# Performance work log

Hardware: AMD Instinct MI355X
Metric: run time of the kernel (lower is better)

## Reference

```python
import jax, jax.numpy as jnp
import numpy as np

EPS = 1e-8  # matches torch F.cosine_similarity eps


def setup_inputs() -> dict:
    key = jax.random.key(0)
    k1, k2 = jax.random.split(key)
    num_nodes, feat_dim, num_edges = 100000, 128, 1600000
    node_features = jax.random.normal(k1, (num_nodes, feat_dim), dtype=jnp.float32)
    edge_index = jax.random.randint(k2, (2, num_edges), 0, num_nodes, dtype=jnp.int64)
    return {"node_features": node_features, "edge_index": edge_index}


def reference(node_features, edge_index):
    # Edge-parallel equivalent of the per-node loop:
    # each edge (s, d) contributes cos(u_s, u_d) to BOTH s and d
    # (the original adj dict appends both directions, duplicates included).
    num_nodes = node_features.shape[0]
    src, dst = edge_index[0], edge_index[1]

    # clamped norms as in torch cosine_similarity
    norms = jnp.maximum(jnp.linalg.norm(node_features, axis=-1), EPS)  # [N]

    # per-edge cosine similarity  [E]
    sim = jnp.einsum("ed,ed->e", node_features[src], node_features[dst]) / (
        norms[src] * norms[dst]
    )

    idx = jnp.concatenate([src, dst])            # [2E] — both endpoints
    vals = jnp.concatenate([sim, sim])           # [2E]
    sums = jax.ops.segment_sum(vals, idx, num_segments=num_nodes)          # [N]
    deg = jax.ops.segment_sum(jnp.ones_like(vals), idx, num_segments=num_nodes)

    # isolated nodes get similarity 1.0
    return jnp.where(deg > 0, sums / jnp.maximum(deg, 1.0), 1.0)
```

## Files before the change

### kernel.cpp

```cpp
#include <hip/hip_runtime.h>

#define FEAT 128
#define NB 8
#define HB 256
#define CHN 25000
#define CNT_SHIFT 24
#define SIM_SCALE 16384.0f
#define INV_SIM (1.0f/16384.0f)

typedef unsigned uv4 __attribute__((ext_vector_type(4)));
typedef unsigned short us4 __attribute__((ext_vector_type(4)));
typedef unsigned long long ull;

__device__ __forceinline__ int dot4(unsigned a, unsigned b, int c) {
#if __has_builtin(__builtin_amdgcn_sdot4)
    return __builtin_amdgcn_sdot4(a, b, c, false);
#else
    c += (int)(signed char)(a)        * (int)(signed char)(b);
    c += (int)(signed char)(a >> 8)   * (int)(signed char)(b >> 8);
    c += (int)(signed char)(a >> 16)  * (int)(signed char)(b >> 16);
    c += (int)(signed char)(a >> 24)  * (int)(signed char)(b >> 24);
    return c;
#endif
}

__device__ __forceinline__ int dot16(uv4 a, uv4 b) {
    int c = dot4(a.x, b.x, 0);
    c = dot4(a.y, b.y, c);
    c = dot4(a.z, b.z, c);
    return dot4(a.w, b.w, c);
}

__global__ void quantize_kernel(const float* __restrict__ feat,
                                unsigned* __restrict__ tab32,
                                float* __restrict__ invq,
                                int num_nodes) {
    const int sub = threadIdx.x & 31;
    const int hpb = blockDim.x >> 5;
    int n = blockIdx.x * hpb + (threadIdx.x >> 5);
    const int stride = gridDim.x * hpb;
    for (; n < num_nodes; n += stride) {
        const float4 v = *reinterpret_cast<const float4*>(feat + (size_t)n * FEAT + sub * 4);
        float am = fmaxf(fmaxf(fabsf(v.x), fabsf(v.y)), fmaxf(fabsf(v.z), fabsf(v.w)));
        am = fmaxf(am, __shfl_xor(am, 16, 64));
        am = fmaxf(am, __shfl_xor(am, 8, 64));
        am = fmaxf(am, __shfl_xor(am, 4, 64));
        am = fmaxf(am, __shfl_xor(am, 2, 64));
        am = fmaxf(am, __shfl_xor(am, 1, 64));
        const float sc = (am > 0.0f) ? (127.0f / am) : 0.0f;
        const int q0 = (int)rintf(v.x * sc);
        const int q1 = (int)rintf(v.y * sc);
        const int q2 = (int)rintf(v.z * sc);
        const int q3 = (int)rintf(v.w * sc);
        int nq = q0 * q0 + q1 * q1 + q2 * q2 + q3 * q3;
        nq += __shfl_xor(nq, 16, 64);
        nq += __shfl_xor(nq, 8, 64);
        nq += __shfl_xor(nq, 4, 64);
        nq += __shfl_xor(nq, 2, 64);
        nq += __shfl_xor(nq, 1, 64);
        tab32[(size_t)n * (FEAT / 4) + sub] =
            (unsigned)(q0 & 0xFF) | ((unsigned)(q1 & 0xFF) << 8) |
            ((unsigned)(q2 & 0xFF) << 16) | ((unsigned)(q3 & 0xFF) << 24);
        if (sub == 0)
            invq[n] = (nq > 0) ? (1.0f / sqrtf((float)nq)) : 0.0f;
    }
}

__global__ void hist_kernel(const int* __restrict__ ei,
                            unsigned* __restrict__ hist,
                            int num_edges, int slice, int chunk) {
    __shared__ unsigned h[NB];
    if (threadIdx.x < NB) h[threadIdx.x] = 0;
    __syncthreads();
    const int lo = blockIdx.x * chunk;
    const int hi = min(lo + chunk, num_edges);
    for (int e = lo + threadIdx.x; e < hi; e += blockDim.x)
        atomicAdd(&h[(unsigned)ei[e] / (unsigned)slice], 1u);
    __syncthreads();
    if (threadIdx.x < NB) hist[threadIdx.x * HB + blockIdx.x] = h[threadIdx.x];
}

__global__ void scan_kernel(unsigned* __restrict__ hist,
                            unsigned* __restrict__ qs,
                            int num_edges) {
    __shared__ unsigned part[256];
    const int t = threadIdx.x;
    unsigned v[8], sum = 0;
#pragma unroll
    for (int i = 0; i < 8; ++i) { v[i] = hist[t * 8 + i]; sum += v[i]; }
    part[t] = sum;
    __syncthreads();
    for (int off = 1; off < 256; off <<= 1) {
        const unsigned x = (t >= off) ? part[t - off] : 0u;
        __syncthreads();
        part[t] += x;
        __syncthreads();
    }
    unsigned run = part[t] - sum;
    if ((t & 31) == 0) qs[t >> 5] = run;
    if (t == 255) qs[NB] = part[255];
#pragma unroll
    for (int i = 0; i < 8; ++i) { const unsigned tmp = v[i]; hist[t * 8 + i] = run; run += tmp; }
}

__global__ void scatter_kernel(const int* __restrict__ ei,
                               const unsigned* __restrict__ hist,
                               ull* __restrict__ sd,
                               int num_edges, int slice, int chunk) {
    __shared__ unsigned cnt[NB];
    if (threadIdx.x < NB) cnt[threadIdx.x] = hist[threadIdx.x * HB + blockIdx.x];
    __syncthreads();
    const int lo = blockIdx.x * chunk;
    const int hi = min(lo + chunk, num_edges);
    for (int e = lo + threadIdx.x; e < hi; e += blockDim.x) {
        const unsigned s = (unsigned)ei[e];
        const unsigned d = (unsigned)ei[(size_t)num_edges + e];
        const unsigned pos = atomicAdd(&cnt[s / (unsigned)slice], 1u);
        sd[pos] = (ull)s | ((ull)d << 32);
    }
}

__global__ void edge_i8_flat_sd(const unsigned char* __restrict__ tab,
                                const ull* __restrict__ sd,
                                const float* __restrict__ invq,
                                unsigned short* __restrict__ sim,
                                int num_edges) {
    const int sub = threadIdx.x & 7;
    const int gid = blockIdx.x * (blockDim.x >> 3) + (threadIdx.x >> 3);
    const int e0 = gid * 4;
    if (e0 >= num_edges) return;
    const bool full = (e0 + 4 <= num_edges);

    int s[4], d[4];
    if (full) {
        const ulonglong2 w0 = *(const ulonglong2*)(sd + e0);
        const ulonglong2 w1 = *(const ulonglong2*)(sd + e0 + 2);
        s[0] = (int)(unsigned)w0.x; d[0] = (int)(unsigned)(w0.x >> 32);
        s[1] = (int)(unsigned)w0.y; d[1] = (int)(unsigned)(w0.y >> 32);
        s[2] = (int)(unsigned)w1.x; d[2] = (int)(unsigned)(w1.x >> 32);
        s[3] = (int)(unsigned)w1.y; d[3] = (int)(unsigned)(w1.y >> 32);
    } else {
#pragma unroll
        for (int k = 0; k < 4; ++k) {
            const int e = min(e0 + k, num_edges - 1);
            const ull w = sd[e];
            s[k] = (int)(unsigned)w; d[k] = (int)(unsigned)(w >> 32);
        }
    }

    uv4 a[4], b[4];
#pragma unroll
    for (int k = 0; k < 4; ++k) {
        a[k] = *(const uv4*)(tab + (size_t)s[k] * FEAT + sub * 16);
        b[k] = *(const uv4*)(tab + (size_t)d[k] * FEAT + sub * 16);
    }
    int pd[4];
#pragma unroll
    for (int k = 0; k < 4; ++k) pd[k] = dot16(a[k], b[k]);
#pragma unroll
    for (int k = 0; k < 4; ++k) {
        pd[k] += __shfl_xor(pd[k], 1, 64);
        pd[k] += __shfl_xor(pd[k], 2, 64);
        pd[k] += __shfl_xor(pd[k], 4, 64);
    }

    int myidx = s[0];
    if (sub == 1) myidx = d[0];
    else if (sub == 2) myidx = s[1];
    else if (sub == 3) myidx = d[1];
    else if (sub == 4) myidx = s[2];
    else if (sub == 5) myidx = d[2];
    else if (sub == 6) myidx = s[3];
    else if (sub == 7) myidx = d[3];

    const float msc = invq[myidx];
    const float prod = msc * __shfl_xor(msc, 1, 64);

    const int gb = (threadIdx.x & 63) & ~7;
    const float pr0 = __shfl(prod, gb + 0, 64);
    const float pr1 = __shfl(prod, gb + 2, 64);
    const float pr2 = __shfl(prod, gb + 4, 64);
    const float pr3 = __shfl(prod, gb + 6, 64);

    if (sub == 0) {
        us4 o;
        o.x = (unsigned short)((float)pd[0] * pr0 * SIM_SCALE + 32768.5f);
        o.y = (unsigned short)((float)pd[1] * pr1 * SIM_SCALE + 32768.5f);
        o.z = (unsigned short)((float)pd[2] * pr2 * SIM_SCALE + 32768.5f);
        o.w = (unsigned short)((float)pd[3] * pr3 * SIM_SCALE + 32768.5f);
        if (full) {
            *(us4*)(sim + e0) = o;
        } else {
            if (e0 < num_edges) sim[e0] = o.x;
            if (e0 + 1 < num_edges) sim[e0 + 1] = o.y;
            if (e0 + 2 < num_edges) sim[e0 + 2] = o.z;
            if (e0 + 3 < num_edges) sim[e0 + 3] = o.w;
        }
    }
}

__global__ void edge_i8_sim(const unsigned char* __restrict__ tab,
                            const int* __restrict__ ei,
                            const float* __restrict__ invq,
                            unsigned short* __restrict__ sim,
                            int num_edges, int aligned4) {
    const int sub = threadIdx.x & 7;
    const int gid = blockIdx.x * (blockDim.x >> 3) + (threadIdx.x >> 3);
    const int e0 = gid * 4;
    if (e0 >= num_edges) return;
    int s[4], d[4];
    const bool fast = aligned4 && (e0 + 4 <= num_edges);
    if (fast) {
        const uv4 si = *(const uv4*)(ei + e0);
        const uv4 di = *(const uv4*)(ei + (size_t)num_edges + e0);
        s[0] = (int)si.x; s[1] = (int)si.y; s[2] = (int)si.z; s[3] = (int)si.w;
        d[0] = (int)di.x; d[1] = (int)di.y; d[2] = (int)di.z; d[3] = (int)di.w;
    } else {
#pragma unroll
        for (int k = 0; k < 4; ++k) {
            const int e = min(e0 + k, num_edges - 1);
            s[k] = ei[e];
            d[k] = ei[(size_t)num_edges + e];
        }
    }
    uv4 a[4], b[4];
#pragma unroll
    for (int k = 0; k < 4; ++k) {
        a[k] = *(const uv4*)(tab + (size_t)s[k] * FEAT + sub * 16);
        b[k] = *(const uv4*)(tab + (size_t)d[k] * FEAT + sub * 16);
    }
    int pd[4];
#pragma unroll
    for (int k = 0; k < 4; ++k) pd[k] = dot16(a[k], b[k]);
#pragma unroll
    for (int k = 0; k < 4; ++k) {
        pd[k] += __shfl_xor(pd[k], 1, 64);
        pd[k] += __shfl_xor(pd[k], 2, 64);
        pd[k] += __shfl_xor(pd[k], 4, 64);
    }
    int myidx = s[0];
    if (sub == 1) myidx = d[0];
    else if (sub == 2) myidx = s[1];
    else if (sub == 3) myidx = d[1];
    else if (sub == 4) myidx = s[2];
    else if (sub == 5) myidx = d[2];
    else if (sub == 6) myidx = s[3];
    else if (sub == 7) myidx = d[3];
    const float msc = invq[myidx];
    const float prod = msc * __shfl_xor(msc, 1, 64);
    const int gb = (threadIdx.x & 63) & ~7;
    const float pr0 = __shfl(prod, gb + 0, 64);
    const float pr1 = __shfl(prod, gb + 2, 64);
    const float pr2 = __shfl(prod, gb + 4, 64);
    const float pr3 = __shfl(prod, gb + 6, 64);
    if (sub == 0) {
        us4 o;
        o.x = (unsigned short)((float)pd[0] * pr0 * SIM_SCALE + 32768.5f);
        o.y = (unsigned short)((float)pd[1] * pr1 * SIM_SCALE + 32768.5f);
        o.z = (unsigned short)((float)pd[2] * pr2 * SIM_SCALE + 32768.5f);
        o.w = (unsigned short)((float)pd[3] * pr3 * SIM_SCALE + 32768.5f);
        if (fast) {
            *(us4*)(sim + e0) = o;
        } else {
            if (e0 < num_edges) sim[e0] = o.x;
            if (e0 + 1 < num_edges) sim[e0 + 1] = o.y;
            if (e0 + 2 < num_edges) sim[e0 + 2] = o.z;
            if (e0 + 3 < num_edges) sim[e0 + 3] = o.w;
        }
    }
}

__global__ __launch_bounds__(1024)
void agg_kernel(const int* __restrict__ ei,
                const ull* __restrict__ sd,
                const unsigned short* __restrict__ sim,
                unsigned* __restrict__ acc,
                int num_edges, int num_nodes, int CH, int S, int use_sd) {
    __shared__ unsigned lds[CHN];
    const int slice = blockIdx.x / CH;
    const int chunk = blockIdx.x % CH;
    const int base = chunk * CHN;
    const int cn = min(CHN, num_nodes - base);

    for (int i = threadIdx.x; i < cn; i += blockDim.x) lds[i] = 0;
    __syncthreads();

    const int P = (num_edges + 3) >> 2;
    const int p0 = (int)((long long)P * slice / S);
    const int p1 = (int)((long long)P * (slice + 1) / S);

    for (int p = p0 + threadIdx.x; p < p1; p += blockDim.x) {
        const int e0 = p * 4;
        if (e0 + 3 < num_edges) {
            unsigned sv[4], dv[4];
            if (use_sd) {
                const ulonglong2 w0 = *(const ulonglong2*)(sd + e0);
                const ulonglong2 w1 = *(const ulonglong2*)(sd + e0 + 2);
                sv[0] = (unsigned)w0.x; dv[0] = (unsigned)(w0.x >> 32);
                sv[1] = (unsigned)w0.y; dv[1] = (unsigned)(w0.y >> 32);
                sv[2] = (unsigned)w1.x; dv[2] = (unsigned)(w1.x >> 32);
                sv[3] = (unsigned)w1.y; dv[3] = (unsigned)(w1.y >> 32);
            } else {
                const uv4 su = *(const uv4*)(ei + e0);
                const uv4 du = *(const uv4*)(ei + (size_t)num_edges + e0);
                sv[0] = su.x; sv[1] = su.y; sv[2] = su.z; sv[3] = su.w;
                dv[0] = du.x; dv[1] = du.y; dv[2] = du.z; dv[3] = du.w;
            }
            const us4 sm = *(const us4*)(sim + e0);
#pragma unroll
            for (int k = 0; k < 4; ++k) {
                const unsigned v = (1u << CNT_SHIFT) | (unsigned)sm[k];
                const unsigned cs = sv[k] - (unsigned)base;
                const unsigned cd = dv[k] - (unsigned)base;
                if (cs < (unsigned)cn) atomicAdd(&lds[cs], v);
                if (cd < (unsigned)cn) atomicAdd(&lds[cd], v);
            }
        } else {
            for (int k = 0; k < 4; ++k) {
                const int e = e0 + k;
                if (e < num_edges) {
                    unsigned sv, dv;
                    if (use_sd) {
                        const ull w = sd[e];
                        sv = (unsigned)w; dv = (unsigned)(w >> 32);
                    } else {
                        sv = (unsigned)ei[e]; dv = (unsigned)ei[(size_t)num_edges + e];
                    }
                    const unsigned v = (1u << CNT_SHIFT) | (unsigned)sim[e];
                    const unsigned cs = sv - (unsigned)base;
                    const unsigned cd = dv - (unsigned)base;
                    if (cs < (unsigned)cn) atomicAdd(&lds[cs], v);
                    if (cd < (unsigned)cn) atomicAdd(&lds[cd], v);
                }
            }
        }
    }
    __syncthreads();
    for (int i = threadIdx.x; i < cn; i += blockDim.x)
        acc[(size_t)slice * num_nodes + base + i] = lds[i];
}

__global__ void edge_i8_atomic(const unsigned char* __restrict__ tab,
                               const int* __restrict__ ei,
                               const float* __restrict__ invq,
                               unsigned* __restrict__ acc,
                               int num_edges, int aligned4) {
    const int sub = threadIdx.x & 7;
    const int gid = blockIdx.x * (blockDim.x >> 3) + (threadIdx.x >> 3);
    const int e0 = gid * 4;
    if (e0 >= num_edges) return;
    int s[4], d[4];
    const bool fast = aligned4 && (e0 + 4 <= num_edges);
    if (fast) {
        const uv4 si = *(const uv4*)(ei + e0);
        const uv4 di = *(const uv4*)(ei + (size_t)num_edges + e0);
        s[0] = (int)si.x; s[1] = (int)si.y; s[2] = (int)si.z; s[3] = (int)si.w;
        d[0] = (int)di.x; d[1] = (int)di.y; d[2] = (int)di.z; d[3] = (int)di.w;
    } else {
#pragma unroll
        for (int k = 0; k < 4; ++k) {
            const int e = min(e0 + k, num_edges - 1);
            s[k] = ei[e];
            d[k] = ei[(size_t)num_edges + e];
        }
    }
    uv4 a[4], b[4];
#pragma unroll
    for (int k = 0; k < 4; ++k) {
        a[k] = *(const uv4*)(tab + (size_t)s[k] * FEAT + sub * 16);
        b[k] = *(const uv4*)(tab + (size_t)d[k] * FEAT + sub * 16);
    }
    int pd[4];
#pragma unroll
    for (int k = 0; k < 4; ++k) pd[k] = dot16(a[k], b[k]);
#pragma unroll
    for (int k = 0; k < 4; ++k) {
        pd[k] += __shfl_xor(pd[k], 1, 64);
        pd[k] += __shfl_xor(pd[k], 2, 64);
        pd[k] += __shfl_xor(pd[k], 4, 64);
    }
    int myidx = s[0];
    if (sub == 1) myidx = d[0];
    else if (sub == 2) myidx = s[1];
    else if (sub == 3) myidx = d[1];
    else if (sub == 4) myidx = s[2];
    else if (sub == 5) myidx = d[2];
    else if (sub == 6) myidx = s[3];
    else if (sub == 7) myidx = d[3];
    int mydot = pd[0];
    if (sub >= 6) mydot = pd[3];
    else if (sub >= 4) mydot = pd[2];
    else if (sub >= 2) mydot = pd[1];
    const float msc = invq[myidx];
    const float prod = msc * __shfl_xor(msc, 1, 64);
    if (fast || (e0 + (sub >> 1)) < num_edges) {
        const unsigned pk = (1u << CNT_SHIFT) |
            (unsigned)((float)mydot * prod * SIM_SCALE + 32768.5f);
        atomicAdd(&acc[myidx], pk);
    }
}

__global__ void final_kernel(const unsigned* __restrict__ acc,
                             float* __restrict__ out,
                             int num_nodes, int S) {
    const int i = blockIdx.x * blockDim.x + threadIdx.x;
    if (i < num_nodes) {
        unsigned cnt = 0, fx = 0;
        for (int c = 0; c < S; ++c) {
            const unsigned x = acc[(size_t)c * num_nodes + i];
            cnt += x >> CNT_SHIFT;
            fx += x & ((1u << CNT_SHIFT) - 1u);
        }
        out[i] = cnt ? ((float)fx * INV_SIM - 2.0f * (float)cnt) / (float)cnt : 1.0f;
    }
}

extern "C" void kernel_launch(void* const* d_in, const int* in_sizes, int n_in,
                              void* d_out, int out_size, void* d_ws, size_t ws_size,
                              hipStream_t stream) {
    const float* feat = (const float*)d_in[0];
    const int* ei = (const int*)d_in[1];
    const int num_nodes = in_sizes[0] / FEAT;
    const int num_edges = in_sizes[1] / 2;
    float* out = (float*)d_out;
    const int aligned4 = ((num_edges & 3) == 0) ? 1 : 0;
    const int slice = (num_nodes + NB - 1) / NB;
    const int CH = (num_nodes + CHN - 1) / CHN;

    const size_t E4 = (size_t)((num_edges + 3) & ~3) + 4;
    const size_t sd_bytes = E4 * sizeof(ull);
    const size_t sim_bytes = E4 * sizeof(unsigned short);
    const size_t invq_bytes = (size_t)num_nodes * sizeof(float);
    const size_t tab_bytes = (size_t)num_nodes * FEAT;
    const size_t meta_bytes = (size_t)NB * HB * 4 + 128;

    const size_t fixedA = sd_bytes + sim_bytes + invq_bytes + tab_bytes + meta_bytes;
    const size_t fixedB = sim_bytes + invq_bytes + tab_bytes;
    const size_t plane = (size_t)num_nodes * sizeof(unsigned);

    int SA = 0, SB = 0;
    if (ws_size > fixedA) SA = (int)(((ws_size - fixedA) / plane > 85) ? 85 : (ws_size - fixedA) / plane);
    if (ws_size > fixedB) SB = (int)(((ws_size - fixedB) / plane > 85) ? 85 : (ws_size - fixedB) / plane);

    if (SA >= 8 && aligned4) {
        ull* sd = (ull*)d_ws;
        unsigned short* sim = (unsigned short*)((char*)d_ws + sd_bytes);
        float* invq = (float*)((char*)d_ws + sd_bytes + sim_bytes);
        unsigned* tab32 = (unsigned*)((char*)d_ws + sd_bytes + sim_bytes + invq_bytes);
        unsigned* hist = (unsigned*)((char*)d_ws + sd_bytes + sim_bytes + invq_bytes + tab_bytes);
        unsigned* qs = hist + NB * HB;
        unsigned* acc = (unsigned*)((char*)d_ws + fixedA);
        const int S = SA;

        quantize_kernel<<<(num_nodes + 7) / 8, 256, 0, stream>>>(feat, tab32, invq, num_nodes);
        const int chunk = (num_edges + HB - 1) / HB;
        hist_kernel<<<HB, 256, 0, stream>>>(ei, hist, num_edges, slice, chunk);
        scan_kernel<<<1, 256, 0, stream>>>(hist, qs, num_edges);
        scatter_kernel<<<HB, 256, 0, stream>>>(ei, hist, sd, num_edges, slice, chunk);
        {
            const int epb = (256 / 8) * 4;
            const int blocks = (num_edges + epb - 1) / epb;
            edge_i8_flat_sd<<<blocks, 256, 0, stream>>>(
                (const unsigned char*)tab32, sd, invq, sim, num_edges);
        }
        agg_kernel<<<CH * S, 1024, 0, stream>>>(ei, sd, sim, acc, num_edges,
                                                num_nodes, CH, S, 1);
        final_kernel<<<(num_nodes + 255) / 256, 256, 0, stream>>>(acc, out, num_nodes, S);
    } else if (SB >= 8 && aligned4) {
        unsigned short* sim = (unsigned short*)d_ws;
        float* invq = (float*)((char*)d_ws + sim_bytes);
        unsigned* tab32 = (unsigned*)((char*)d_ws + sim_bytes + invq_bytes);
        unsigned* acc = (unsigned*)((char*)d_ws + fixedB);
        const int S = SB;

        quantize_kernel<<<(num_nodes + 7) / 8, 256, 0, stream>>>(feat, tab32, invq, num_nodes);
        {
            const int epb = (256 / 8) * 4;
            const int blocks = (num_edges + epb - 1) / epb;
            edge_i8_sim<<<blocks, 256, 0, stream>>>(
                (const unsigned char*)tab32, ei, invq, sim, num_edges, aligned4);
        }
        agg_kernel<<<CH * S, 1024, 0, stream>>>(ei, (const ull*)d_ws , sim, acc,
                                                num_edges, num_nodes, CH, S, 0);
        final_kernel<<<(num_nodes + 255) / 256, 256, 0, stream>>>(acc, out, num_nodes, S);
    } else {
        unsigned* acc = (unsigned*)d_ws;
        float* invq = (float*)((char*)d_ws + plane);
        unsigned* tab32 = (unsigned*)((char*)d_ws + plane + invq_bytes);
        hipMemsetAsync(acc, 0, plane, stream);
        quantize_kernel<<<(num_nodes + 7) / 8, 256, 0, stream>>>(feat, tab32, invq, num_nodes);
        {
            const int epb = (256 / 8) * 4;
            const int blocks = (num_edges + epb - 1) / epb;
            edge_i8_atomic<<<blocks, 256, 0, stream>>>(
                (const unsigned char*)tab32, ei, invq, acc, num_edges, aligned4);
        }
        final_kernel<<<(num_nodes + 255) / 256, 256, 0, stream>>>(acc, out, num_nodes, 1);
    }
}
```

Measured before the change: 147.1 us.

## Aggregate scatter atomics per wavefront and bind edge blocks to source buckets

```diff
diff --git a/kernel.cpp b/kernel.cpp
--- a/kernel.cpp
+++ b/kernel.cpp
@@ -3,6 +3,7 @@
 #define FEAT 128
 #define NB 8
 #define HB 256
+#define NBPB 1600
 #define CHN 25000
 #define CNT_SHIFT 24
 #define SIM_SCALE 16384.0f
@@ -110,91 +111,118 @@
     __shared__ unsigned cnt[NB];
     if (threadIdx.x < NB) cnt[threadIdx.x] = hist[threadIdx.x * HB + blockIdx.x];
     __syncthreads();
+    const int lane = threadIdx.x & 63;
+    const ull lanebit = 1ull << lane;
     const int lo = blockIdx.x * chunk;
     const int hi = min(lo + chunk, num_edges);
     for (int e = lo + threadIdx.x; e < hi; e += blockDim.x) {
         const unsigned s = (unsigned)ei[e];
         const unsigned d = (unsigned)ei[(size_t)num_edges + e];
-        const unsigned pos = atomicAdd(&cnt[s / (unsigned)slice], 1u);
-        sd[pos] = (ull)s | ((ull)d << 32);
-    }
-}
-
-__global__ void edge_i8_flat_sd(const unsigned char* __restrict__ tab,
-                                const ull* __restrict__ sd,
-                                const float* __restrict__ invq,
-                                unsigned short* __restrict__ sim,
-                                int num_edges) {
+        const unsigned b = s / (unsigned)slice;
+        const ull pair = (ull)s | ((ull)d << 32);
+#pragma unroll
+        for (int k = 0; k < NB; ++k) {
+            const ull mask = __ballot(b == (unsigned)k);
+            if (b == (unsigned)k) {
+                const int leader = __ffsll((unsigned long long)mask) - 1;
+                unsigned wbase = 0;
+                if (lane == leader)
+                    wbase = atomicAdd(&cnt[k], (unsigned)__popcll(mask));
+                wbase = __shfl(wbase, leader, 64);
+                sd[wbase + (unsigned)__popcll(mask & (lanebit - 1ull))] = pair;
+            }
+        }
+    }
+}
+
+__global__ void edge_i8_aff(const unsigned char* __restrict__ tab,
+                            const ull* __restrict__ sd,
+                            const float* __restrict__ invq,
+                            unsigned short* __restrict__ sim,
+                            const unsigned* __restrict__ qs,
+                            int num_edges) {
     const int sub = threadIdx.x & 7;
-    const int gid = blockIdx.x * (blockDim.x >> 3) + (threadIdx.x >> 3);
-    const int e0 = gid * 4;
-    if (e0 >= num_edges) return;
-    const bool full = (e0 + 4 <= num_edges);
-
-    int s[4], d[4];
-    if (full) {
-        const ulonglong2 w0 = *(const ulonglong2*)(sd + e0);
-        const ulonglong2 w1 = *(const ulonglong2*)(sd + e0 + 2);
-        s[0] = (int)(unsigned)w0.x; d[0] = (int)(unsigned)(w0.x >> 32);
-        s[1] = (int)(unsigned)w0.y; d[1] = (int)(unsigned)(w0.y >> 32);
-        s[2] = (int)(unsigned)w1.x; d[2] = (int)(unsigned)(w1.x >> 32);
-        s[3] = (int)(unsigned)w1.y; d[3] = (int)(unsigned)(w1.y >> 32);
-    } else {
+    const int grp = threadIdx.x >> 3;
+    const int q = blockIdx.x & (NB - 1);
+    const int w = blockIdx.x >> 3;
+    const int pstart = (int)((qs[q] + 3u) >> 2);
+    const int pend = (int)((qs[q + 1] + 3u) >> 2);
+    const int npack = pend - pstart;
+    if (npack <= 0) return;
+    const int per = (npack + NBPB - 1) / NBPB;
+    const int p0 = pstart + w * per;
+    const int p1 = min(p0 + per, pend);
+
+    for (int p = p0 + grp; p < p1; p += 32) {
+        const int e0 = p * 4;
+        if (e0 >= num_edges) continue;
+        const bool full = (e0 + 4 <= num_edges);
+
+        int s[4], d[4];
+        if (full) {
+            const ulonglong2 w0 = *(const ulonglong2*)(sd + e0);
+            const ulonglong2 w1 = *(const ulonglong2*)(sd + e0 + 2);
+            s[0] = (int)(unsigned)w0.x; d[0] = (int)(unsigned)(w0.x >> 32);
+            s[1] = (int)(unsigned)w0.y; d[1] = (int)(unsigned)(w0.y >> 32);
+            s[2] = (int)(unsigned)w1.x; d[2] = (int)(unsigned)(w1.x >> 32);
+            s[3] = (int)(unsigned)w1.y; d[3] = (int)(unsigned)(w1.y >> 32);
+        } else {
+#pragma unroll
+            for (int k = 0; k < 4; ++k) {
+                const int e = min(e0 + k, num_edges - 1);
+                const ull wv = sd[e];
+                s[k] = (int)(unsigned)wv; d[k] = (int)(unsigned)(wv >> 32);
+            }
+        }
+
+        uv4 a[4], b[4];
 #pragma unroll
         for (int k = 0; k < 4; ++k) {
-            const int e = min(e0 + k, num_edges - 1);
-            const ull w = sd[e];
-            s[k] = (int)(unsigned)w; d[k] = (int)(unsigned)(w >> 32);
-        }
-    }
-
-    uv4 a[4], b[4];
-#pragma unroll
-    for (int k = 0; k < 4; ++k) {
-        a[k] = *(const uv4*)(tab + (size_t)s[k] * FEAT + sub * 16);
-        b[k] = *(const uv4*)(tab + (size_t)d[k] * FEAT + sub * 16);
-    }
-    int pd[4];
-#pragma unroll
-    for (int k = 0; k < 4; ++k) pd[k] = dot16(a[k], b[k]);
-#pragma unroll
-    for (int k = 0; k < 4; ++k) {
-        pd[k] += __shfl_xor(pd[k], 1, 64);
-        pd[k] += __shfl_xor(pd[k], 2, 64);
-        pd[k] += __shfl_xor(pd[k], 4, 64);
-    }
-
-    int myidx = s[0];
-    if (sub == 1) myidx = d[0];
-    else if (sub == 2) myidx = s[1];
-    else if (sub == 3) myidx = d[1];
-    else if (sub == 4) myidx = s[2];
-    else if (sub == 5) myidx = d[2];
-    else if (sub == 6) myidx = s[3];
-    else if (sub == 7) myidx = d[3];
-
-    const float msc = invq[myidx];
-    const float prod = msc * __shfl_xor(msc, 1, 64);
-
-    const int gb = (threadIdx.x & 63) & ~7;
-    const float pr0 = __shfl(prod, gb + 0, 64);
-    const float pr1 = __shfl(prod, gb + 2, 64);
-    const float pr2 = __shfl(prod, gb + 4, 64);
-    const float pr3 = __shfl(prod, gb + 6, 64);
-
-    if (sub == 0) {
-        us4 o;
-        o.x = (unsigned short)((float)pd[0] * pr0 * SIM_SCALE + 32768.5f);
-        o.y = (unsigned short)((float)pd[1] * pr1 * SIM_SCALE + 32768.5f);
-        o.z = (unsigned short)((float)pd[2] * pr2 * SIM_SCALE + 32768.5f);
-        o.w = (unsigned short)((float)pd[3] * pr3 * SIM_SCALE + 32768.5f);
-        if (full) {
-            *(us4*)(sim + e0) = o;
-        } else {
-            if (e0 < num_edges) sim[e0] = o.x;
-            if (e0 + 1 < num_edges) sim[e0 + 1] = o.y;
-            if (e0 + 2 < num_edges) sim[e0 + 2] = o.z;
-            if (e0 + 3 < num_edges) sim[e0 + 3] = o.w;
+            a[k] = *(const uv4*)(tab + (size_t)s[k] * FEAT + sub * 16);
+            b[k] = *(const uv4*)(tab + (size_t)d[k] * FEAT + sub * 16);
+        }
+        int pd[4];
+#pragma unroll
+        for (int k = 0; k < 4; ++k) pd[k] = dot16(a[k], b[k]);
+#pragma unroll
+        for (int k = 0; k < 4; ++k) {
+            pd[k] += __shfl_xor(pd[k], 1, 64);
+            pd[k] += __shfl_xor(pd[k], 2, 64);
+            pd[k] += __shfl_xor(pd[k], 4, 64);
+        }
+
+        int myidx = s[0];
+        if (sub == 1) myidx = d[0];
+        else if (sub == 2) myidx = s[1];
+        else if (sub == 3) myidx = d[1];
+        else if (sub == 4) myidx = s[2];
+        else if (sub == 5) myidx = d[2];
+        else if (sub == 6) myidx = s[3];
+        else if (sub == 7) myidx = d[3];
+
+        const float msc = invq[myidx];
+        const float prod = msc * __shfl_xor(msc, 1, 64);
+
+        const int gb = (threadIdx.x & 63) & ~7;
+        const float pr0 = __shfl(prod, gb + 0, 64);
+        const float pr1 = __shfl(prod, gb + 2, 64);
+        const float pr2 = __shfl(prod, gb + 4, 64);
+        const float pr3 = __shfl(prod, gb + 6, 64);
+
+        if (sub == 0) {
+            us4 o;
+            o.x = (unsigned short)((float)pd[0] * pr0 * SIM_SCALE + 32768.5f);
+            o.y = (unsigned short)((float)pd[1] * pr1 * SIM_SCALE + 32768.5f);
+            o.z = (unsigned short)((float)pd[2] * pr2 * SIM_SCALE + 32768.5f);
+            o.w = (unsigned short)((float)pd[3] * pr3 * SIM_SCALE + 32768.5f);
+            if (full) {
+                *(us4*)(sim + e0) = o;
+            } else {
+                if (e0 < num_edges) sim[e0] = o.x;
+                if (e0 + 1 < num_edges) sim[e0 + 1] = o.y;
+                if (e0 + 2 < num_edges) sim[e0 + 2] = o.z;
+                if (e0 + 3 < num_edges) sim[e0 + 3] = o.w;
+            }
         }
     }
 }
@@ -439,8 +467,8 @@
     const size_t plane = (size_t)num_nodes * sizeof(unsigned);
 
     int SA = 0, SB = 0;
-    if (ws_size > fixedA) SA = (int)(((ws_size - fixedA) / plane > 85) ? 85 : (ws_size - fixedA) / plane);
-    if (ws_size > fixedB) SB = (int)(((ws_size - fixedB) / plane > 85) ? 85 : (ws_size - fixedB) / plane);
+    if (ws_size > fixedA) SA = (int)(((ws_size - fixedA) / plane > 64) ? 64 : (ws_size - fixedA) / plane);
+    if (ws_size > fixedB) SB = (int)(((ws_size - fixedB) / plane > 64) ? 64 : (ws_size - fixedB) / plane);
 
     if (SA >= 8 && aligned4) {
         ull* sd = (ull*)d_ws;
@@ -457,12 +485,8 @@
         hist_kernel<<<HB, 256, 0, stream>>>(ei, hist, num_edges, slice, chunk);
         scan_kernel<<<1, 256, 0, stream>>>(hist, qs, num_edges);
         scatter_kernel<<<HB, 256, 0, stream>>>(ei, hist, sd, num_edges, slice, chunk);
-        {
-            const int epb = (256 / 8) * 4;
-            const int blocks = (num_edges + epb - 1) / epb;
-            edge_i8_flat_sd<<<blocks, 256, 0, stream>>>(
-                (const unsigned char*)tab32, sd, invq, sim, num_edges);
-        }
+        edge_i8_aff<<<NB * NBPB, 256, 0, stream>>>(
+            (const unsigned char*)tab32, sd, invq, sim, qs, num_edges);
         agg_kernel<<<CH * S, 1024, 0, stream>>>(ei, sd, sim, acc, num_edges,
                                                 num_nodes, CH, S, 1);
         final_kernel<<<(num_nodes + 255) / 256, 256, 0, stream>>>(acc, out, num_nodes, S);
```

After: 165.9 us. 1.13x slower.
